# Optimization experiments

Hardware: AMD Instinct MI355X
Metric: run time of the kernel (lower is better)

The kernel has to match this reference:

```python
import jax, jax.numpy as jnp
import numpy as np

N, E = 20000, 5000
IN_FT, OUT_FT = 128, 128
DENSITY = 0.01  # fraction of nonzeros in the incidence matrix


def setup_inputs() -> dict:
    key = jax.random.key(0)
    kx, kh, kw, kb = jax.random.split(key, 4)
    X = jax.random.normal(kx, (N, IN_FT), dtype=jnp.float32)
    H = (jax.random.uniform(kh, (N, E)) < DENSITY).astype(jnp.float32)
    # xavier_normal_ with gain=0.01
    xav_std = 0.01 * np.sqrt(2.0 / (IN_FT + OUT_FT))
    weight_trans = jax.random.normal(kw, (IN_FT, OUT_FT), dtype=jnp.float32) * xav_std
    bias = jax.random.normal(kb, (OUT_FT,), dtype=jnp.float32) * 0.01
    return {"X": X, "H": H, "weight_trans": weight_trans, "bias": bias}


def reference(X, H, weight_trans, bias):
    # X: [N, in_ft], H: [N, E] incidence
    Xw = X @ weight_trans                      # [N, out_ft]
    DV = jnp.sum(H, axis=1) + 1e-12            # node degrees, [N]
    DE = jnp.sum(H, axis=0) + 1e-12            # hyperedge degrees, [E]
    # G = diag(1/DV) @ H @ diag(1/DE) @ H^T applied to Xw, computed in the
    # efficient order without materializing the NxN matrix G:
    M = H.T @ Xw                               # [E, out_ft]
    M = M / DE[:, None]                        # diag(1/DE) scaling
    out = H @ M                                # [N, out_ft]
    out = out / DV[:, None]                    # diag(1/DV) scaling
    out = out + bias
    return jax.nn.relu(out)
```

## Files before the change

kernel.cpp:

```cpp
#include <hip/hip_runtime.h>
#include <hip/hip_bf16.h>

#define N_NODES 20000
#define N_EDGES 5000
#define FT 128
#define NP 20
#define ROW_U64 80
#define N_CHUNKS 63
#define CH_ROWS 320
#define SEG 24
#define SEG_STRIDE 1536
#define MAX_DEG 320

__global__ __launch_bounds__(256) void x_to_bf16(
    const float2* __restrict__ X2, __hip_bfloat162* __restrict__ Xb2) {
  int i = blockIdx.x * 256 + threadIdx.x;
  Xb2[i] = __float22bfloat162_rn(X2[i]);
}

__global__ __launch_bounds__(64) void scan_fused(
    const float4* __restrict__ H4,
    unsigned long long* __restrict__ Hbt,
    int* __restrict__ seg,
    int* __restrict__ scnt) {
  const int lane  = threadIdx.x;
  const int chunk = blockIdx.x / NP;
  const int panel = blockIdx.x % NP;
  const int idx4  = panel * 64 + lane;
  const bool lvalid = idx4 < 1250;
  const int r0   = chunk * CH_ROWS;
  const int rend = min(r0 + CH_ROWS, N_NODES);
  const int c0   = idx4 * 4;

  int cnt0 = 0, cnt1 = 0, cnt2 = 0, cnt3 = 0;
  int* sp0 = seg + (size_t)(c0 + 0) * SEG_STRIDE + chunk * SEG;
  int* sp1 = sp0 + SEG_STRIDE;
  int* sp2 = sp1 + SEG_STRIDE;
  int* sp3 = sp2 + SEG_STRIDE;

  for (int g64 = r0; g64 < rend; g64 += 64) {
    unsigned long long m0 = 0ull, m1 = 0ull, m2 = 0ull, m3 = 0ull;
    const int gend = min(g64 + 64, rend);
    for (int rb = g64; rb < gend; rb += 8) {
      float4 vv[8];
#pragma unroll
      for (int k = 0; k < 8; ++k) vv[k] = make_float4(0.f, 0.f, 0.f, 0.f);
      if (lvalid) {
        const float4* bp = H4 + (size_t)rb * 1250 + idx4;
#pragma unroll
        for (int k = 0; k < 8; ++k) vv[k] = bp[(size_t)k * 1250];
      }
#pragma unroll
      for (int k = 0; k < 8; ++k) {
        const int r = rb + k;
        unsigned long long b0 = __ballot(vv[k].x != 0.f);
        unsigned long long b1 = __ballot(vv[k].y != 0.f);
        unsigned long long b2 = __ballot(vv[k].z != 0.f);
        unsigned long long b3 = __ballot(vv[k].w != 0.f);
        const bool keep = (lane == (r & 63));
        m0 = keep ? b0 : m0;  m1 = keep ? b1 : m1;
        m2 = keep ? b2 : m2;  m3 = keep ? b3 : m3;
        if (vv[k].x != 0.f) { if (cnt0 < SEG) sp0[cnt0] = r; ++cnt0; }
        if (vv[k].y != 0.f) { if (cnt1 < SEG) sp1[cnt1] = r; ++cnt1; }
        if (vv[k].z != 0.f) { if (cnt2 < SEG) sp2[cnt2] = r; ++cnt2; }
        if (vv[k].w != 0.f) { if (cnt3 < SEG) sp3[cnt3] = r; ++cnt3; }
      }
    }
    const int rr = g64 + lane;
    if (rr < gend) {
      unsigned long long* hp = Hbt + (size_t)rr * ROW_U64 + panel * 4;
      hp[0] = m0; hp[1] = m1; hp[2] = m2; hp[3] = m3;
    }
  }
  scnt[(c0 + 0) * 64 + chunk] = min(cnt0, SEG);
  scnt[(c0 + 1) * 64 + chunk] = min(cnt1, SEG);
  scnt[(c0 + 2) * 64 + chunk] = min(cnt2, SEG);
  scnt[(c0 + 3) * 64 + chunk] = min(cnt3, SEG);
}

__global__ __launch_bounds__(256) void edge_gather(
    const __hip_bfloat162* __restrict__ Xb2,
    const int* __restrict__ seg, const int* __restrict__ scnt,
    float2* __restrict__ P2, int* __restrict__ de) {
  __shared__ int sidx[4][MAX_DEG];
  const int wid = threadIdx.x >> 6, lane = threadIdx.x & 63;
  const int e = blockIdx.x * 4 + wid;

  int cl = (lane < N_CHUNKS) ? scnt[e * 64 + lane] : 0;
  cl = min(cl, SEG);
  int off = cl;
  for (int d = 1; d < 64; d <<= 1) {
    int t = __shfl_up(off, d);
    if (lane >= d) off += t;
  }
  int total = __shfl(off, N_CHUNKS - 1);
  off -= cl;
  if (cl > 0) {
    const int* sb = seg + (size_t)e * SEG_STRIDE + lane * SEG;
    for (int i = 0; i < cl; ++i) {
      int o = off + i;
      if (o < MAX_DEG) sidx[wid][o] = sb[i];
    }
  }
  __builtin_amdgcn_s_waitcnt(0);
  int t = min(total, MAX_DEG);

  float sx = 0.f, sy = 0.f;
  int g = 0;
  for (; g + 16 <= t; g += 16) {
    int nn[16];
#pragma unroll
    for (int q = 0; q < 16; ++q) nn[q] = sidx[wid][g + q];
    float2 aa[16];
#pragma unroll
    for (int q = 0; q < 16; ++q) aa[q] = __bfloat1622float2(Xb2[nn[q] * 64 + lane]);
#pragma unroll
    for (int q = 0; q < 16; ++q) { sx += aa[q].x; sy += aa[q].y; }
  }
  for (; g < t; ++g) {
    float2 a = __bfloat1622float2(Xb2[sidx[wid][g] * 64 + lane]);
    sx += a.x; sy += a.y;
  }
  P2[e * 64 + lane] = make_float2(sx, sy);
  if (lane == 0) de[e] = total;
}

__global__ __launch_bounds__(256) void gemm_M(
    const float* __restrict__ P, const float* __restrict__ W,
    const int* __restrict__ de, float* __restrict__ M) {
  int f = threadIdx.x & (FT - 1);
  int half = threadIdx.x >> 7;
  int base = blockIdx.x * 16 + half * 8;
#pragma unroll
  for (int g = 0; g < 8; g += 4) {
    int e = base + g;
    if (e >= N_EDGES) break;
    const float* p0 = P + (e + 0) * FT;
    const float* p1 = P + (e + 1) * FT;
    const float* p2 = P + (e + 2) * FT;
    const float* p3 = P + (e + 3) * FT;
    float a0 = 0.f, a1 = 0.f, a2 = 0.f, a3 = 0.f;
#pragma unroll 4
    for (int k = 0; k < FT; ++k) {
      float w = W[k * FT + f];
      a0 += p0[k] * w; a1 += p1[k] * w; a2 += p2[k] * w; a3 += p3[k] * w;
    }
    M[(e + 0) * FT + f] = a0 / ((float)de[e + 0] + 1e-12f);
    M[(e + 1) * FT + f] = a1 / ((float)de[e + 1] + 1e-12f);
    M[(e + 2) * FT + f] = a2 / ((float)de[e + 2] + 1e-12f);
    M[(e + 3) * FT + f] = a3 / ((float)de[e + 3] + 1e-12f);
  }
}

__global__ __launch_bounds__(256) void row_apply(
    const unsigned long long* __restrict__ Hbt,
    const float2* __restrict__ M2, const float2* __restrict__ bias2,
    float2* __restrict__ out2) {
  const int wid = threadIdx.x >> 6, lane = threadIdx.x & 63;
  const int n = blockIdx.x * 4 + wid;
  unsigned long long m_lo = Hbt[(size_t)n * ROW_U64 + lane];
  unsigned long long m_hi = (lane < ROW_U64 - 64)
      ? Hbt[(size_t)n * ROW_U64 + 64 + lane] : 0ull;
  float sx = 0.f, sy = 0.f;
  int dv = 0;
  for (int vp = 0; vp < ROW_U64; ++vp) {
    unsigned long long mp = (vp < 64) ? __shfl(m_lo, vp) : __shfl(m_hi, vp - 64);
    if (mp == 0ull) continue;
    dv += __popcll(mp);
    int ebase = (vp >> 2) * 256 + (vp & 3);
    while (mp) {
      int b0 = __ffsll(mp) - 1; mp &= mp - 1;
      if (mp) {
        int b1 = __ffsll(mp) - 1; mp &= mp - 1;
        float2 u = M2[(size_t)(ebase + 4 * b0) * 64 + lane];
        float2 w = M2[(size_t)(ebase + 4 * b1) * 64 + lane];
        sx += u.x + w.x; sy += u.y + w.y;
      } else {
        float2 u = M2[(size_t)(ebase + 4 * b0) * 64 + lane];
        sx += u.x; sy += u.y;
      }
    }
  }
  float inv = 1.f / ((float)dv + 1e-12f);
  float2 bb = bias2[lane];
  float2 o;
  o.x = fmaxf(fmaf(sx, inv, bb.x), 0.f);
  o.y = fmaxf(fmaf(sy, inv, bb.y), 0.f);
  out2[(size_t)n * 64 + lane] = o;
}

extern "C" void kernel_launch(void* const* d_in, const int* in_sizes, int n_in,
                              void* d_out, int out_size, void* d_ws, size_t ws_size,
                              hipStream_t stream) {
  const float* X    = (const float*)d_in[0];
  const float* H    = (const float*)d_in[1];
  const float* W    = (const float*)d_in[2];
  const float* bias = (const float*)d_in[3];
  float* out = (float*)d_out;

  int* ws = (int*)d_ws;
  int* seg                = ws;
  int* scnt               = ws + 7864320;
  unsigned long long* Hbt = (unsigned long long*)(ws + 8192000);
  __hip_bfloat162* Xb2    = (__hip_bfloat162*)(ws + 11392000);
  float* P                = (float*)(ws + 12672000);
  int* de                 = ws + 13312000;
  float* M                = (float*)(ws + 13317120);

  x_to_bf16  <<<5000, 256, 0, stream>>>((const float2*)X, Xb2);
  scan_fused <<<NP * N_CHUNKS, 64, 0, stream>>>((const float4*)H, Hbt, seg, scnt);
  edge_gather<<<1250, 256, 0, stream>>>(Xb2, seg, scnt, (float2*)P, de);
  gemm_M     <<<(N_EDGES + 15) / 16, 256, 0, stream>>>(P, W, de, M);
  row_apply  <<<5000, 256, 0, stream>>>(Hbt, (const float2*)M,
                                        (const float2*)bias, (float2*)out);
}
```

Measured before the change: 698.5 us.

## Replace per-column segment index lists with transposed bitmask for edge gather

The scan kernel no longer writes per-chunk row index segments with divergent per-lane stores. It now builds a transposed column bitmask (HbtT) via a 64x64 ballot transpose inside each wave, and launches one block per 64-row group instead of per 320-row chunk. The edge_gather kernel decodes node indices from that bitmask with popcount, prefix scan and ffs, in place of reading the segment lists. This drops the scattered index writes and the SEG=24 per-chunk cap, at the cost of 256 extra ballots per wave and more blocks.

```diff
diff --git a/kernel.cpp b/kernel.cpp
--- a/kernel.cpp
+++ b/kernel.cpp
@@ -1,15 +1,15 @@
 #include <hip/hip_runtime.h>
 #include <hip/hip_bf16.h>
+
+typedef unsigned long long u64;
 
 #define N_NODES 20000
 #define N_EDGES 5000
 #define FT 128
-#define NP 20
+#define NT 20
+#define NRG 313
 #define ROW_U64 80
-#define N_CHUNKS 63
-#define CH_ROWS 320
-#define SEG 24
-#define SEG_STRIDE 1536
+#define COL_U64 320
 #define MAX_DEG 320
 
 __global__ __launch_bounds__(256) void x_to_bf16(
@@ -18,96 +18,102 @@
   Xb2[i] = __float22bfloat162_rn(X2[i]);
 }
 
-__global__ __launch_bounds__(64) void scan_fused(
+__global__ __launch_bounds__(64) void scan_bitmask(
     const float4* __restrict__ H4,
-    unsigned long long* __restrict__ Hbt,
-    int* __restrict__ seg,
-    int* __restrict__ scnt) {
-  const int lane  = threadIdx.x;
-  const int chunk = blockIdx.x / NP;
-  const int panel = blockIdx.x % NP;
-  const int idx4  = panel * 64 + lane;
-  const bool lvalid = idx4 < 1250;
-  const int r0   = chunk * CH_ROWS;
-  const int rend = min(r0 + CH_ROWS, N_NODES);
-  const int c0   = idx4 * 4;
-
-  int cnt0 = 0, cnt1 = 0, cnt2 = 0, cnt3 = 0;
-  int* sp0 = seg + (size_t)(c0 + 0) * SEG_STRIDE + chunk * SEG;
-  int* sp1 = sp0 + SEG_STRIDE;
-  int* sp2 = sp1 + SEG_STRIDE;
-  int* sp3 = sp2 + SEG_STRIDE;
-
-  for (int g64 = r0; g64 < rend; g64 += 64) {
-    unsigned long long m0 = 0ull, m1 = 0ull, m2 = 0ull, m3 = 0ull;
-    const int gend = min(g64 + 64, rend);
-    for (int rb = g64; rb < gend; rb += 8) {
-      float4 vv[8];
-#pragma unroll
-      for (int k = 0; k < 8; ++k) vv[k] = make_float4(0.f, 0.f, 0.f, 0.f);
-      if (lvalid) {
-        const float4* bp = H4 + (size_t)rb * 1250 + idx4;
-#pragma unroll
-        for (int k = 0; k < 8; ++k) vv[k] = bp[(size_t)k * 1250];
-      }
-#pragma unroll
-      for (int k = 0; k < 8; ++k) {
-        const int r = rb + k;
-        unsigned long long b0 = __ballot(vv[k].x != 0.f);
-        unsigned long long b1 = __ballot(vv[k].y != 0.f);
-        unsigned long long b2 = __ballot(vv[k].z != 0.f);
-        unsigned long long b3 = __ballot(vv[k].w != 0.f);
-        const bool keep = (lane == (r & 63));
-        m0 = keep ? b0 : m0;  m1 = keep ? b1 : m1;
-        m2 = keep ? b2 : m2;  m3 = keep ? b3 : m3;
-        if (vv[k].x != 0.f) { if (cnt0 < SEG) sp0[cnt0] = r; ++cnt0; }
-        if (vv[k].y != 0.f) { if (cnt1 < SEG) sp1[cnt1] = r; ++cnt1; }
-        if (vv[k].z != 0.f) { if (cnt2 < SEG) sp2[cnt2] = r; ++cnt2; }
-        if (vv[k].w != 0.f) { if (cnt3 < SEG) sp3[cnt3] = r; ++cnt3; }
-      }
-    }
-    const int rr = g64 + lane;
-    if (rr < gend) {
-      unsigned long long* hp = Hbt + (size_t)rr * ROW_U64 + panel * 4;
-      hp[0] = m0; hp[1] = m1; hp[2] = m2; hp[3] = m3;
-    }
-  }
-  scnt[(c0 + 0) * 64 + chunk] = min(cnt0, SEG);
-  scnt[(c0 + 1) * 64 + chunk] = min(cnt1, SEG);
-  scnt[(c0 + 2) * 64 + chunk] = min(cnt2, SEG);
-  scnt[(c0 + 3) * 64 + chunk] = min(cnt3, SEG);
+    u64* __restrict__ Hbt,
+    u64* __restrict__ HbtT) {
+  const int lane = threadIdx.x;
+  const int t  = blockIdx.x % NT;
+  const int rg = blockIdx.x / NT;
+  const int r0 = rg * 64;
+  const int rows = min(64, N_NODES - r0);
+  const int idx4 = t * 64 + lane;
+  const bool lv = idx4 < 1250;
+
+  u64 m0 = 0, m1 = 0, m2 = 0, m3 = 0;
+  for (int kb = 0; kb < rows; kb += 8) {
+    float4 vv[8];
+#pragma unroll
+    for (int k = 0; k < 8; ++k) vv[k] = make_float4(0.f, 0.f, 0.f, 0.f);
+    if (lv) {
+      const float4* bp = H4 + (size_t)(r0 + kb) * 1250 + idx4;
+#pragma unroll
+      for (int k = 0; k < 8; ++k) vv[k] = bp[(size_t)k * 1250];
+    }
+#pragma unroll
+    for (int k = 0; k < 8; ++k) {
+      u64 b0 = __ballot(vv[k].x != 0.f);
+      u64 b1 = __ballot(vv[k].y != 0.f);
+      u64 b2 = __ballot(vv[k].z != 0.f);
+      u64 b3 = __ballot(vv[k].w != 0.f);
+      const bool keep = (lane == kb + k);
+      m0 = keep ? b0 : m0;  m1 = keep ? b1 : m1;
+      m2 = keep ? b2 : m2;  m3 = keep ? b3 : m3;
+    }
+  }
+  if (lane < rows) {
+    u64* hp = Hbt + (size_t)(r0 + lane) * ROW_U64 + t * 4;
+    hp[0] = m0; hp[1] = m1; hp[2] = m2; hp[3] = m3;
+  }
+  u64 t0 = 0, t1 = 0, t2 = 0, t3 = 0;
+  for (int l = 0; l < 64; ++l) {
+    u64 c0 = __ballot((m0 >> l) & 1ull);
+    u64 c1 = __ballot((m1 >> l) & 1ull);
+    u64 c2 = __ballot((m2 >> l) & 1ull);
+    u64 c3 = __ballot((m3 >> l) & 1ull);
+    const bool keep = (lane == l);
+    t0 = keep ? c0 : t0;  t1 = keep ? c1 : t1;
+    t2 = keep ? c2 : t2;  t3 = keep ? c3 : t3;
+  }
+  const int c = t * 256 + 4 * lane;
+  HbtT[(size_t)(c + 0) * COL_U64 + rg] = t0;
+  HbtT[(size_t)(c + 1) * COL_U64 + rg] = t1;
+  HbtT[(size_t)(c + 2) * COL_U64 + rg] = t2;
+  HbtT[(size_t)(c + 3) * COL_U64 + rg] = t3;
 }
 
 __global__ __launch_bounds__(256) void edge_gather(
     const __hip_bfloat162* __restrict__ Xb2,
-    const int* __restrict__ seg, const int* __restrict__ scnt,
+    const u64* __restrict__ HbtT,
     float2* __restrict__ P2, int* __restrict__ de) {
   __shared__ int sidx[4][MAX_DEG];
   const int wid = threadIdx.x >> 6, lane = threadIdx.x & 63;
   const int e = blockIdx.x * 4 + wid;
 
-  int cl = (lane < N_CHUNKS) ? scnt[e * 64 + lane] : 0;
-  cl = min(cl, SEG);
-  int off = cl;
+  const u64* cb = HbtT + (size_t)e * COL_U64;
+  u64 cm[5];
+#pragma unroll
+  for (int q = 0; q < 5; ++q) {
+    int u = q * 64 + lane;
+    cm[q] = (u < NRG) ? cb[u] : 0ull;
+  }
+  int cnt = 0;
+#pragma unroll
+  for (int q = 0; q < 5; ++q) cnt += __popcll(cm[q]);
+  int off = cnt;
   for (int d = 1; d < 64; d <<= 1) {
-    int t = __shfl_up(off, d);
-    if (lane >= d) off += t;
-  }
-  int total = __shfl(off, N_CHUNKS - 1);
-  off -= cl;
-  if (cl > 0) {
-    const int* sb = seg + (size_t)e * SEG_STRIDE + lane * SEG;
-    for (int i = 0; i < cl; ++i) {
-      int o = off + i;
-      if (o < MAX_DEG) sidx[wid][o] = sb[i];
+    int v = __shfl_up(off, d);
+    if (lane >= d) off += v;
+  }
+  int total = __shfl(off, 63);
+  off -= cnt;
+#pragma unroll
+  for (int q = 0; q < 5; ++q) {
+    u64 w = cm[q];
+    int rbase = q * 4096 + lane * 64;
+    while (w) {
+      int b = __ffsll(w) - 1;
+      w &= w - 1;
+      if (off < MAX_DEG) sidx[wid][off] = rbase + b;
+      ++off;
     }
   }
   __builtin_amdgcn_s_waitcnt(0);
-  int t = min(total, MAX_DEG);
+  int tt = min(total, MAX_DEG);
 
   float sx = 0.f, sy = 0.f;
   int g = 0;
-  for (; g + 16 <= t; g += 16) {
+  for (; g + 16 <= tt; g += 16) {
     int nn[16];
 #pragma unroll
     for (int q = 0; q < 16; ++q) nn[q] = sidx[wid][g + q];
@@ -117,7 +123,7 @@
 #pragma unroll
     for (int q = 0; q < 16; ++q) { sx += aa[q].x; sy += aa[q].y; }
   }
-  for (; g < t; ++g) {
+  for (; g < tt; ++g) {
     float2 a = __bfloat1622float2(Xb2[sidx[wid][g] * 64 + lane]);
     sx += a.x; sy += a.y;
   }
@@ -153,18 +159,17 @@
 }
 
 __global__ __launch_bounds__(256) void row_apply(
-    const unsigned long long* __restrict__ Hbt,
+    const u64* __restrict__ Hbt,
     const float2* __restrict__ M2, const float2* __restrict__ bias2,
     float2* __restrict__ out2) {
   const int wid = threadIdx.x >> 6, lane = threadIdx.x & 63;
   const int n = blockIdx.x * 4 + wid;
-  unsigned long long m_lo = Hbt[(size_t)n * ROW_U64 + lane];
-  unsigned long long m_hi = (lane < ROW_U64 - 64)
-      ? Hbt[(size_t)n * ROW_U64 + 64 + lane] : 0ull;
+  u64 m_lo = Hbt[(size_t)n * ROW_U64 + lane];
+  u64 m_hi = (lane < ROW_U64 - 64) ? Hbt[(size_t)n * ROW_U64 + 64 + lane] : 0ull;
   float sx = 0.f, sy = 0.f;
   int dv = 0;
   for (int vp = 0; vp < ROW_U64; ++vp) {
-    unsigned long long mp = (vp < 64) ? __shfl(m_lo, vp) : __shfl(m_hi, vp - 64);
+    u64 mp = (vp < 64) ? __shfl(m_lo, vp) : __shfl(m_hi, vp - 64);
     if (mp == 0ull) continue;
     dv += __popcll(mp);
     int ebase = (vp >> 2) * 256 + (vp & 3);
@@ -199,18 +204,17 @@
   float* out = (float*)d_out;
 
   int* ws = (int*)d_ws;
-  int* seg                = ws;
-  int* scnt               = ws + 7864320;
-  unsigned long long* Hbt = (unsigned long long*)(ws + 8192000);
-  __hip_bfloat162* Xb2    = (__hip_bfloat162*)(ws + 11392000);
-  float* P                = (float*)(ws + 12672000);
-  int* de                 = ws + 13312000;
-  float* M                = (float*)(ws + 13317120);
-
-  x_to_bf16  <<<5000, 256, 0, stream>>>((const float2*)X, Xb2);
-  scan_fused <<<NP * N_CHUNKS, 64, 0, stream>>>((const float4*)H, Hbt, seg, scnt);
-  edge_gather<<<1250, 256, 0, stream>>>(Xb2, seg, scnt, (float2*)P, de);
-  gemm_M     <<<(N_EDGES + 15) / 16, 256, 0, stream>>>(P, W, de, M);
-  row_apply  <<<5000, 256, 0, stream>>>(Hbt, (const float2*)M,
-                                        (const float2*)bias, (float2*)out);
-}
+  u64* Hbt             = (u64*)ws;
+  u64* HbtT            = (u64*)(ws + 3200000);
+  __hip_bfloat162* Xb2 = (__hip_bfloat162*)(ws + 6476800);
+  float* P             = (float*)(ws + 7756800);
+  int* de              = ws + 8396800;
+  float* M             = (float*)(ws + 8401920);
+
+  x_to_bf16   <<<5000, 256, 0, stream>>>((const float2*)X, Xb2);
+  scan_bitmask<<<NRG * NT, 64, 0, stream>>>((const float4*)H, Hbt, HbtT);
+  edge_gather <<<1250, 256, 0, stream>>>(Xb2, HbtT, (float2*)P, de);
+  gemm_M      <<<(N_EDGES + 15) / 16, 256, 0, stream>>>(P, W, de, M);
+  row_apply   <<<5000, 256, 0, stream>>>(Hbt, (const float2*)M,
+                                         (const float2*)bias, (float2*)out);
+}
```

Result: faster. 674.0 us (-3.5%).
